# Kernel tuning notes

Hardware: AMD Instinct MI355X
Metric: run time of the kernel (lower is better)

The kernel has to match this reference:

```python
import jax, jax.numpy as jnp
import numpy as np

N_NODES = 100000
D_IN = 64
HIDDEN = 64
OUT = 1
N_EDGES = 1000000


def setup_inputs() -> dict:
    key = jax.random.key(0)
    ks = jax.random.split(key, 10)
    s = 1.0 / np.sqrt(D_IN)
    x = jax.random.normal(ks[0], (N_NODES, D_IN), dtype=jnp.float32)
    edge_index = jax.random.randint(ks[1], (2, N_EDGES), 0, N_NODES, dtype=jnp.int64)
    return {
        "x": x,
        "edge_index": edge_index,
        # SAGEConv layer 1: lin_l (on aggregated neighbors, with bias), lin_r (on root)
        "W1_l": jax.random.uniform(ks[2], (D_IN, HIDDEN), jnp.float32, -s, s),
        "W1_r": jax.random.uniform(ks[3], (D_IN, HIDDEN), jnp.float32, -s, s),
        "b1": jnp.zeros((HIDDEN,), jnp.float32),
        # SAGEConv layer 2
        "W2_l": jax.random.uniform(ks[4], (HIDDEN, HIDDEN), jnp.float32, -s, s),
        "W2_r": jax.random.uniform(ks[5], (HIDDEN, HIDDEN), jnp.float32, -s, s),
        "b2": jnp.zeros((HIDDEN,), jnp.float32),
        # final classifier
        "Wc": jax.random.uniform(ks[6], (HIDDEN, OUT), jnp.float32, -s, s),
        "bc": jnp.zeros((OUT,), jnp.float32),
    }


def _sage_conv(x, src, dst, W_l, W_r, b):
    # mean aggregation of source-node features onto destination nodes
    n = x.shape[0]
    agg = jax.ops.segment_sum(x[src], dst, num_segments=n)          # [N, d]
    cnt = jax.ops.segment_sum(jnp.ones_like(dst, dtype=x.dtype), dst, num_segments=n)
    mean = agg / jnp.maximum(cnt, 1.0)[:, None]
    # PyG SAGEConv: out = lin_l(mean_neighbors) + lin_r(x)
    return mean @ W_l + x @ W_r + b


def reference(x, edge_index, W1_l, W1_r, b1, W2_l, W2_r, b2, Wc, bc):
    src, dst = edge_index[0], edge_index[1]
    h = jax.nn.relu(_sage_conv(x, src, dst, W1_l, W1_r, b1))
    # dropout is identity in eval mode
    h = jax.nn.relu(_sage_conv(h, src, dst, W2_l, W2_r, b2))
    return h @ Wc + bc  # [N, 1] logits
```

## Files before the change

### kernel.cpp

```cpp
#include <hip/hip_runtime.h>

#define N_NODES 100000
#define D 64
#define N_EDGES 1000000

__global__ __launch_bounds__(256) void count_kernel(
    const int* __restrict__ dst, int* __restrict__ cnt) {
    int t = blockIdx.x * blockDim.x + threadIdx.x;
    int nt = gridDim.x * blockDim.x;
    for (int e = t; e < N_EDGES; e += nt) atomicAdd(&cnt[dst[e]], 1);
}

__global__ __launch_bounds__(256) void scan_kernel(
    const int* __restrict__ cnt, int* __restrict__ offset,
    int* __restrict__ wcur, int* __restrict__ total) {
    int n = blockIdx.x * blockDim.x + threadIdx.x;
    int lane = threadIdx.x & 63;
    int c = (n < N_NODES) ? cnt[n] : 0;
    int pre = c;
#pragma unroll
    for (int off = 1; off < 64; off <<= 1) {
        int t = __shfl_up(pre, off);
        if (lane >= off) pre += t;
    }
    int base = 0;
    if (lane == 63) base = atomicAdd(total, pre);
    base = __shfl(base, 63);
    if (n < N_NODES) {
        int o = base + pre - c;
        offset[n] = o;
        wcur[n] = o;
    }
}

__global__ __launch_bounds__(256) void fill_kernel(
    const int* __restrict__ src, const int* __restrict__ dst,
    int* __restrict__ wcur, int* __restrict__ binned) {
    int t = blockIdx.x * blockDim.x + threadIdx.x;
    int nt = gridDim.x * blockDim.x;
    for (int e = t; e < N_EDGES; e += nt) {
        int pos = atomicAdd(&wcur[dst[e]], 1);
        binned[pos] = src[e];
    }
}

__global__ __launch_bounds__(256) void agg_kernel(
    const float* __restrict__ feat, const int* __restrict__ binned,
    const int* __restrict__ offset, const int* __restrict__ cnt,
    float* __restrict__ mean_out) {
    int wave = (blockIdx.x * blockDim.x + threadIdx.x) >> 6;
    int lane = threadIdx.x & 63;
    int nw = (gridDim.x * blockDim.x) >> 6;
    for (int n = wave; n < N_NODES; n += nw) {
        int c = cnt[n];
        int o = offset[n];
        float a0 = 0.f, a1 = 0.f, a2 = 0.f, a3 = 0.f;
        int i = 0;
        for (; i + 3 < c; i += 4) {
            int s0 = binned[o + i], s1 = binned[o + i + 1];
            int s2 = binned[o + i + 2], s3 = binned[o + i + 3];
            a0 += feat[((size_t)s0 << 6) + lane];
            a1 += feat[((size_t)s1 << 6) + lane];
            a2 += feat[((size_t)s2 << 6) + lane];
            a3 += feat[((size_t)s3 << 6) + lane];
        }
        for (; i < c; ++i) a0 += feat[((size_t)binned[o + i] << 6) + lane];
        float m = (a0 + a1) + (a2 + a3);
        m = (c > 0) ? m / (float)c : 0.f;
        mean_out[((size_t)n << 6) + lane] = m;
    }
}

template <bool FUSE_OUT>
__global__ __launch_bounds__(256) void transform_kernel(
    const float* __restrict__ mean, const float* __restrict__ xin,
    const float* __restrict__ Wl, const float* __restrict__ Wr,
    const float* __restrict__ bias,
    const float* __restrict__ Wc, const float* __restrict__ bc,
    float* __restrict__ out) {
    int lane = threadIdx.x & 63;

    float wl[64], wr[64];
#pragma unroll
    for (int k = 0; k < 64; ++k) {
        wl[k] = Wl[k * 64 + lane];
        wr[k] = Wr[k * 64 + lane];
    }
    float bj = bias[lane];
    float wcj = FUSE_OUT ? Wc[lane] : 0.f;
    float bcv = FUSE_OUT ? bc[0] : 0.f;

    int wave = (blockIdx.x * blockDim.x + threadIdx.x) >> 6;
    int nwaves = (gridDim.x * blockDim.x) >> 6;
    for (int n = wave; n < N_NODES; n += nwaves) {
        const float4* mrow = (const float4*)(mean + ((size_t)n << 6));
        const float4* xrow = (const float4*)(xin + ((size_t)n << 6));
        float am = 0.f, ax = 0.f;
#pragma unroll
        for (int ci = 0; ci < 16; ++ci) {
            float4 mv = mrow[ci];
            float4 xv = xrow[ci];
            am = fmaf(mv.x, wl[4 * ci + 0], am);
            am = fmaf(mv.y, wl[4 * ci + 1], am);
            am = fmaf(mv.z, wl[4 * ci + 2], am);
            am = fmaf(mv.w, wl[4 * ci + 3], am);
            ax = fmaf(xv.x, wr[4 * ci + 0], ax);
            ax = fmaf(xv.y, wr[4 * ci + 1], ax);
            ax = fmaf(xv.z, wr[4 * ci + 2], ax);
            ax = fmaf(xv.w, wr[4 * ci + 3], ax);
        }
        float acc = fmaxf(am + ax + bj, 0.f);
        if (FUSE_OUT) {
            float v = acc * wcj;
#pragma unroll
            for (int off = 32; off; off >>= 1) v += __shfl_xor(v, off);
            if (lane == 0) out[n] = v + bcv;
        } else {
            out[((size_t)n << 6) + lane] = acc;
        }
    }
}

extern "C" void kernel_launch(void* const* d_in, const int* in_sizes, int n_in,
                              void* d_out, int out_size, void* d_ws, size_t ws_size,
                              hipStream_t stream) {
    const float* x   = (const float*)d_in[0];
    const int* ei    = (const int*)d_in[1];
    const float* W1l = (const float*)d_in[2];
    const float* W1r = (const float*)d_in[3];
    const float* b1  = (const float*)d_in[4];
    const float* W2l = (const float*)d_in[5];
    const float* W2r = (const float*)d_in[6];
    const float* b2  = (const float*)d_in[7];
    const float* Wc  = (const float*)d_in[8];
    const float* bc  = (const float*)d_in[9];
    float* out = (float*)d_out;

    const int* src = ei;
    const int* dst = ei + N_EDGES;

    char* w = (char*)d_ws;
    int*   cnt     = (int*)w;      w += (size_t)N_NODES * 4;
    int*   total   = (int*)w;      w += 16 * 4;
    int*   offset  = (int*)w;      w += (size_t)N_NODES * 4;
    int*   wcur    = (int*)w;      w += (size_t)N_NODES * 4;
    int*   binned  = (int*)w;      w += (size_t)N_EDGES * 4;
    float* meanbuf = (float*)w;    w += (size_t)N_NODES * D * 4;
    float* h1      = (float*)w;

    hipMemsetAsync(cnt, 0, ((size_t)N_NODES + 16) * 4, stream);
    count_kernel<<<2048, 256, 0, stream>>>(dst, cnt);
    scan_kernel<<<(N_NODES + 255) / 256, 256, 0, stream>>>(cnt, offset, wcur, total);
    fill_kernel<<<2048, 256, 0, stream>>>(src, dst, wcur, binned);

    agg_kernel<<<2048, 256, 0, stream>>>(x, binned, offset, cnt, meanbuf);
    transform_kernel<false><<<1024, 256, 0, stream>>>(
        meanbuf, x, W1l, W1r, b1, nullptr, nullptr, h1);

    agg_kernel<<<2048, 256, 0, stream>>>(h1, binned, offset, cnt, meanbuf);
    transform_kernel<true><<<1024, 256, 0, stream>>>(
        meanbuf, h1, W2l, W2r, b2, Wc, bc, out);
}
```

Measured before the change: 659.3 us.

## Split dual-matmul transform into two single-weight kernels to cut register pressure

The fused transform kernel kept two 64-float weight columns per lane in registers. It is replaced by two kernels: one multiplies the aggregated mean by W_l in place, and a second multiplies the root features by W_r and adds the partial result, bias and ReLU. Each kernel holds one weight column, which targets higher occupancy (launch_bounds 256,3, grid doubled). The cost is an extra kernel launch per layer and an extra 25.6 MB write and read of the intermediate buffer.

```diff
diff --git a/kernel.cpp b/kernel.cpp
--- a/kernel.cpp
+++ b/kernel.cpp
@@ -71,52 +71,76 @@
     }
 }
 
+__global__ __launch_bounds__(256, 3) void matA_kernel(
+    float* __restrict__ buf, const float* __restrict__ W) {
+    int lane = threadIdx.x & 63;
+    float wcol[64];
+#pragma unroll
+    for (int k = 0; k < 64; ++k) wcol[k] = W[k * 64 + lane];
+
+    int wave = (blockIdx.x * blockDim.x + threadIdx.x) >> 6;
+    int nw = (gridDim.x * blockDim.x) >> 6;
+    for (int n = wave; n < N_NODES; n += nw) {
+        const float4* row = (const float4*)(buf + ((size_t)n << 6));
+        float acc0 = 0.f, acc1 = 0.f;
+#pragma unroll
+        for (int c = 0; c < 16; c += 2) {
+            float4 v0 = row[c];
+            float4 v1 = row[c + 1];
+            acc0 = fmaf(v0.x, wcol[4 * c + 0], acc0);
+            acc0 = fmaf(v0.y, wcol[4 * c + 1], acc0);
+            acc0 = fmaf(v0.z, wcol[4 * c + 2], acc0);
+            acc0 = fmaf(v0.w, wcol[4 * c + 3], acc0);
+            acc1 = fmaf(v1.x, wcol[4 * c + 4], acc1);
+            acc1 = fmaf(v1.y, wcol[4 * c + 5], acc1);
+            acc1 = fmaf(v1.z, wcol[4 * c + 6], acc1);
+            acc1 = fmaf(v1.w, wcol[4 * c + 7], acc1);
+        }
+        buf[((size_t)n << 6) + lane] = acc0 + acc1;
+    }
+}
+
 template <bool FUSE_OUT>
-__global__ __launch_bounds__(256) void transform_kernel(
-    const float* __restrict__ mean, const float* __restrict__ xin,
-    const float* __restrict__ Wl, const float* __restrict__ Wr,
-    const float* __restrict__ bias,
+__global__ __launch_bounds__(256, 3) void matB_kernel(
+    const float* __restrict__ acc_in, const float* __restrict__ xin,
+    const float* __restrict__ W, const float* __restrict__ bias,
     const float* __restrict__ Wc, const float* __restrict__ bc,
     float* __restrict__ out) {
     int lane = threadIdx.x & 63;
-
-    float wl[64], wr[64];
+    float wcol[64];
 #pragma unroll
-    for (int k = 0; k < 64; ++k) {
-        wl[k] = Wl[k * 64 + lane];
-        wr[k] = Wr[k * 64 + lane];
-    }
+    for (int k = 0; k < 64; ++k) wcol[k] = W[k * 64 + lane];
     float bj = bias[lane];
     float wcj = FUSE_OUT ? Wc[lane] : 0.f;
     float bcv = FUSE_OUT ? bc[0] : 0.f;
 
     int wave = (blockIdx.x * blockDim.x + threadIdx.x) >> 6;
-    int nwaves = (gridDim.x * blockDim.x) >> 6;
-    for (int n = wave; n < N_NODES; n += nwaves) {
-        const float4* mrow = (const float4*)(mean + ((size_t)n << 6));
-        const float4* xrow = (const float4*)(xin + ((size_t)n << 6));
-        float am = 0.f, ax = 0.f;
+    int nw = (gridDim.x * blockDim.x) >> 6;
+    for (int n = wave; n < N_NODES; n += nw) {
+        float a = acc_in[((size_t)n << 6) + lane];
+        const float4* row = (const float4*)(xin + ((size_t)n << 6));
+        float acc0 = a + bj, acc1 = 0.f;
 #pragma unroll
-        for (int ci = 0; ci < 16; ++ci) {
-            float4 mv = mrow[ci];
-            float4 xv = xrow[ci];
-            am = fmaf(mv.x, wl[4 * ci + 0], am);
-            am = fmaf(mv.y, wl[4 * ci + 1], am);
-            am = fmaf(mv.z, wl[4 * ci + 2], am);
-            am = fmaf(mv.w, wl[4 * ci + 3], am);
-            ax = fmaf(xv.x, wr[4 * ci + 0], ax);
-            ax = fmaf(xv.y, wr[4 * ci + 1], ax);
-            ax = fmaf(xv.z, wr[4 * ci + 2], ax);
-            ax = fmaf(xv.w, wr[4 * ci + 3], ax);
+        for (int c = 0; c < 16; c += 2) {
+            float4 v0 = row[c];
+            float4 v1 = row[c + 1];
+            acc0 = fmaf(v0.x, wcol[4 * c + 0], acc0);
+            acc0 = fmaf(v0.y, wcol[4 * c + 1], acc0);
+            acc0 = fmaf(v0.z, wcol[4 * c + 2], acc0);
+            acc0 = fmaf(v0.w, wcol[4 * c + 3], acc0);
+            acc1 = fmaf(v1.x, wcol[4 * c + 4], acc1);
+            acc1 = fmaf(v1.y, wcol[4 * c + 5], acc1);
+            acc1 = fmaf(v1.z, wcol[4 * c + 6], acc1);
+            acc1 = fmaf(v1.w, wcol[4 * c + 7], acc1);
         }
-        float acc = fmaxf(am + ax + bj, 0.f);
+        float h = fmaxf(acc0 + acc1, 0.f);
         if (FUSE_OUT) {
-            float v = acc * wcj;
+            float v = h * wcj;
 #pragma unroll
             for (int off = 32; off; off >>= 1) v += __shfl_xor(v, off);
             if (lane == 0) out[n] = v + bcv;
         } else {
-            out[((size_t)n << 6) + lane] = acc;
+            out[((size_t)n << 6) + lane] = h;
         }
     }
 }
@@ -154,10 +178,12 @@
     fill_kernel<<<2048, 256, 0, stream>>>(src, dst, wcur, binned);
 
     agg_kernel<<<2048, 256, 0, stream>>>(x, binned, offset, cnt, meanbuf);
-    transform_kernel<false><<<1024, 256, 0, stream>>>(
-        meanbuf, x, W1l, W1r, b1, nullptr, nullptr, h1);
+    matA_kernel<<<2048, 256, 0, stream>>>(meanbuf, W1l);
+    matB_kernel<false><<<2048, 256, 0, stream>>>(
+        meanbuf, x, W1r, b1, nullptr, nullptr, h1);
 
     agg_kernel<<<2048, 256, 0, stream>>>(h1, binned, offset, cnt, meanbuf);
-    transform_kernel<true><<<1024, 256, 0, stream>>>(
-        meanbuf, h1, W2l, W2r, b2, Wc, bc, out);
+    matA_kernel<<<2048, 256, 0, stream>>>(meanbuf, W2l);
+    matB_kernel<true><<<2048, 256, 0, stream>>>(
+        meanbuf, h1, W2r, b2, Wc, bc, out);
 }
```

New measurement: 600.9 us. 8.9% less time.

## Tile transform kernel through LDS with 32-node blocks and staged weight columns

Applied to the files above, without the earlier changes.

The transform kernel now stages a 32-node tile of mean and root features into shared memory with coalesced float4 loads. Each wave computes 8 nodes, loading Wl and Wr columns one after the other instead of holding both in registers, and launch bounds request 4 blocks per SM. The goal is to cut register pressure so occupancy rises, and to replace the per-lane uncoalesced row reads with LDS broadcasts. In exchange, weights are reloaded for every block, 3125 blocks are launched instead of a persistent grid, and there is no tail handling, which relies on N_NODES dividing evenly by 32.

```diff
diff --git a/kernel.cpp b/kernel.cpp
--- a/kernel.cpp
+++ b/kernel.cpp
@@ -3,6 +3,8 @@
 #define N_NODES 100000
 #define D 64
 #define N_EDGES 1000000
+#define TILE 32
+#define NTILES (N_NODES / TILE)
 
 __global__ __launch_bounds__(256) void count_kernel(
     const int* __restrict__ dst, int* __restrict__ cnt) {
@@ -72,51 +74,90 @@
 }
 
 template <bool FUSE_OUT>
-__global__ __launch_bounds__(256) void transform_kernel(
+__global__ __launch_bounds__(256, 4) void transform_kernel(
     const float* __restrict__ mean, const float* __restrict__ xin,
     const float* __restrict__ Wl, const float* __restrict__ Wr,
     const float* __restrict__ bias,
     const float* __restrict__ Wc, const float* __restrict__ bc,
     float* __restrict__ out) {
-    int lane = threadIdx.x & 63;
-
-    float wl[64], wr[64];
-#pragma unroll
-    for (int k = 0; k < 64; ++k) {
-        wl[k] = Wl[k * 64 + lane];
-        wr[k] = Wr[k * 64 + lane];
-    }
+    __shared__ float sm[TILE * D];
+    __shared__ float sx[TILE * D];
+    int tid = threadIdx.x;
+    int lane = tid & 63, wave = tid >> 6;
+    int tile = blockIdx.x;
+
+    const float4* gm = (const float4*)mean + (size_t)tile * (TILE * D / 4);
+    const float4* gx = (const float4*)xin + (size_t)tile * (TILE * D / 4);
+    ((float4*)sm)[tid] = gm[tid];
+    ((float4*)sm)[tid + 256] = gm[tid + 256];
+    ((float4*)sx)[tid] = gx[tid];
+    ((float4*)sx)[tid + 256] = gx[tid + 256];
+
     float bj = bias[lane];
     float wcj = FUSE_OUT ? Wc[lane] : 0.f;
     float bcv = FUSE_OUT ? bc[0] : 0.f;
-
-    int wave = (blockIdx.x * blockDim.x + threadIdx.x) >> 6;
-    int nwaves = (gridDim.x * blockDim.x) >> 6;
-    for (int n = wave; n < N_NODES; n += nwaves) {
-        const float4* mrow = (const float4*)(mean + ((size_t)n << 6));
-        const float4* xrow = (const float4*)(xin + ((size_t)n << 6));
-        float am = 0.f, ax = 0.f;
-#pragma unroll
-        for (int ci = 0; ci < 16; ++ci) {
-            float4 mv = mrow[ci];
-            float4 xv = xrow[ci];
-            am = fmaf(mv.x, wl[4 * ci + 0], am);
-            am = fmaf(mv.y, wl[4 * ci + 1], am);
-            am = fmaf(mv.z, wl[4 * ci + 2], am);
-            am = fmaf(mv.w, wl[4 * ci + 3], am);
-            ax = fmaf(xv.x, wr[4 * ci + 0], ax);
-            ax = fmaf(xv.y, wr[4 * ci + 1], ax);
-            ax = fmaf(xv.z, wr[4 * ci + 2], ax);
-            ax = fmaf(xv.w, wr[4 * ci + 3], ax);
-        }
-        float acc = fmaxf(am + ax + bj, 0.f);
+    __syncthreads();
+
+    float acc[8];
+    {
+        float wcol[64];
+#pragma unroll
+        for (int k = 0; k < 64; ++k) wcol[k] = Wl[k * 64 + lane];
+#pragma unroll
+        for (int mm = 0; mm < 8; ++mm) {
+            const float4* row = (const float4*)(sm + (wave * 8 + mm) * D);
+            float a0 = 0.f, a1 = 0.f;
+#pragma unroll
+            for (int c = 0; c < 16; c += 2) {
+                float4 v0 = row[c];
+                float4 v1 = row[c + 1];
+                a0 = fmaf(v0.x, wcol[4 * c + 0], a0);
+                a0 = fmaf(v0.y, wcol[4 * c + 1], a0);
+                a0 = fmaf(v0.z, wcol[4 * c + 2], a0);
+                a0 = fmaf(v0.w, wcol[4 * c + 3], a0);
+                a1 = fmaf(v1.x, wcol[4 * c + 4], a1);
+                a1 = fmaf(v1.y, wcol[4 * c + 5], a1);
+                a1 = fmaf(v1.z, wcol[4 * c + 6], a1);
+                a1 = fmaf(v1.w, wcol[4 * c + 7], a1);
+            }
+            acc[mm] = a0 + a1;
+        }
+    }
+    {
+        float wcol[64];
+#pragma unroll
+        for (int k = 0; k < 64; ++k) wcol[k] = Wr[k * 64 + lane];
+#pragma unroll
+        for (int mm = 0; mm < 8; ++mm) {
+            const float4* row = (const float4*)(sx + (wave * 8 + mm) * D);
+            float a0 = 0.f, a1 = 0.f;
+#pragma unroll
+            for (int c = 0; c < 16; c += 2) {
+                float4 v0 = row[c];
+                float4 v1 = row[c + 1];
+                a0 = fmaf(v0.x, wcol[4 * c + 0], a0);
+                a0 = fmaf(v0.y, wcol[4 * c + 1], a0);
+                a0 = fmaf(v0.z, wcol[4 * c + 2], a0);
+                a0 = fmaf(v0.w, wcol[4 * c + 3], a0);
+                a1 = fmaf(v1.x, wcol[4 * c + 4], a1);
+                a1 = fmaf(v1.y, wcol[4 * c + 5], a1);
+                a1 = fmaf(v1.z, wcol[4 * c + 6], a1);
+                a1 = fmaf(v1.w, wcol[4 * c + 7], a1);
+            }
+            acc[mm] += a0 + a1;
+        }
+    }
+#pragma unroll
+    for (int mm = 0; mm < 8; ++mm) {
+        int n = tile * TILE + wave * 8 + mm;
+        float h = fmaxf(acc[mm] + bj, 0.f);
         if (FUSE_OUT) {
-            float v = acc * wcj;
+            float v = h * wcj;
 #pragma unroll
             for (int off = 32; off; off >>= 1) v += __shfl_xor(v, off);
             if (lane == 0) out[n] = v + bcv;
         } else {
-            out[((size_t)n << 6) + lane] = acc;
+            out[((size_t)n << 6) + lane] = h;
         }
     }
 }
@@ -154,10 +195,10 @@
     fill_kernel<<<2048, 256, 0, stream>>>(src, dst, wcur, binned);
 
     agg_kernel<<<2048, 256, 0, stream>>>(x, binned, offset, cnt, meanbuf);
-    transform_kernel<false><<<1024, 256, 0, stream>>>(
+    transform_kernel<false><<<NTILES, 256, 0, stream>>>(
         meanbuf, x, W1l, W1r, b1, nullptr, nullptr, h1);
 
     agg_kernel<<<2048, 256, 0, stream>>>(h1, binned, offset, cnt, meanbuf);
-    transform_kernel<true><<<1024, 256, 0, stream>>>(
+    transform_kernel<true><<<NTILES, 256, 0, stream>>>(
         meanbuf, h1, W2l, W2r, b2, Wc, bc, out);
 }
```

Result: slower. 1.807 ms (+174.0%).
